# Kernel tuning notes

Measured on AMD Instinct MI355X. Metric: run time of the kernel, lower is better.

The kernel has to match this reference:

```python
import jax, jax.numpy as jnp
import numpy as np

B, L, H, D = 2, 2048, 16, 64
HID = H * D
EPS = 1e-6


def setup_inputs() -> dict:
    key = jax.random.key(0)
    k1, k2, k3 = jax.random.split(key, 3)
    x = jax.random.normal(k1, (B, L, HID), dtype=jnp.float32)
    Wqkv = jax.random.normal(k2, (HID, 3 * HID), dtype=jnp.float32) * 0.02
    Wo = jax.random.normal(k3, (HID, HID), dtype=jnp.float32) * 0.02
    q_norm_w = jnp.ones((D,), dtype=jnp.float32)
    k_norm_w = jnp.ones((D,), dtype=jnp.float32)
    # real RoPE tables: (L, D/2)
    d2 = D // 2
    inv_freq = 1.0 / (10000.0 ** (np.arange(d2, dtype=np.float32) / d2))
    ang = np.arange(L, dtype=np.float32)[:, None] * inv_freq[None, :]
    cos = jnp.asarray(np.cos(ang), dtype=jnp.float32)
    sin = jnp.asarray(np.sin(ang), dtype=jnp.float32)
    return {"x": x, "Wqkv": Wqkv, "Wo": Wo, "q_norm_w": q_norm_w,
            "k_norm_w": k_norm_w, "cos": cos, "sin": sin}


def _rmsnorm(t, w, eps=EPS):
    # normalize over last (head_dim) axis
    var = jnp.mean(t * t, axis=-1, keepdims=True)
    return t * jax.lax.rsqrt(var + eps) * w


def _rope(t, cos, sin):
    # t: (B,H,L,D); cos,sin: (1,1,L,D/2)
    d2 = t.shape[-1] // 2
    t1, t2 = t[..., :d2], t[..., d2:]
    return jnp.concatenate([t1 * cos - t2 * sin, t1 * sin + t2 * cos], axis=-1)


def reference(x, Wqkv, Wo, q_norm_w, k_norm_w, cos, sin):
    Bx, Lx, _ = x.shape
    qkv = x @ Wqkv                                   # (B,L,3*HID)
    qkv = qkv.reshape(Bx, Lx, 3, H, D)
    q = jnp.transpose(qkv[:, :, 0], (0, 2, 1, 3))    # (B,H,L,D)
    k = jnp.transpose(qkv[:, :, 1], (0, 2, 1, 3))
    v = jnp.transpose(qkv[:, :, 2], (0, 2, 1, 3))
    q = _rmsnorm(q, q_norm_w)
    k = _rmsnorm(k, k_norm_w)
    c = cos[:Lx][None, None]                         # (1,1,L,D/2)
    s = sin[:Lx][None, None]
    q = _rope(q, c, s)
    k = _rope(k, c, s)
    scale = 1.0 / jnp.sqrt(jnp.float32(D))
    scores = jnp.einsum("bhqd,bhkd->bhqk", q, k) * scale
    causal = jnp.tril(jnp.ones((Lx, Lx), dtype=bool))
    scores = jnp.where(causal, scores, jnp.finfo(scores.dtype).min)
    attn = jax.nn.softmax(scores, axis=-1)
    out = jnp.einsum("bhqk,bhkd->bhqd", attn, v)     # (B,H,L,D)
    out = jnp.transpose(out, (0, 2, 1, 3)).reshape(Bx, Lx, HID)
    return out @ Wo
```

## Files before the change

### kernel.cpp

```cpp
#include <hip/hip_runtime.h>
#include <hip/hip_bf16.h>

typedef __attribute__((ext_vector_type(8))) short bh8;
typedef __attribute__((ext_vector_type(4))) float f4;

typedef unsigned short u16;
typedef unsigned int u32;

__device__ inline u16 f2b(float f) {
  __hip_bfloat16 h = __float2bfloat16(f);
  union { __hip_bfloat16 h; u16 u; } v; v.h = h; return v.u;
}
__device__ inline float b2f(u16 b) {
  union { u32 u; float f; } v; v.u = ((u32)b) << 16;
  return v.f;
}

__device__ __forceinline__ void gload16(const u16* g, u16* l) {
  __builtin_amdgcn_global_load_lds(
      (__attribute__((address_space(1))) void*)(g),
      (__attribute__((address_space(3))) void*)(l),
      16, 0, 0);
}

__global__ __launch_bounds__(256) void k_prep1(const float* __restrict__ x,
                                               const float* __restrict__ Wqkv,
                                               const float* __restrict__ Wo,
                                               u16* __restrict__ xb,
                                               u16* __restrict__ wqkvT,
                                               u16* __restrict__ woT) {
  int idx = blockIdx.x;
  if (idx < 4096) {
    int i = (idx * 256 + threadIdx.x) * 4;
    float4 v = *(const float4*)&x[i];
    ushort4 o;
    o.x = f2b(v.x); o.y = f2b(v.y); o.z = f2b(v.z); o.w = f2b(v.w);
    *(ushort4*)&xb[i] = o;
    return;
  }
  __shared__ u16 t[32][33];
  const float* W; u16* WT; int K, N, bxi, byi;
  if (idx < 7168) {
    int id2 = idx - 4096;
    W = Wqkv; WT = wqkvT; K = 1024; N = 3072;
    bxi = id2 % 96; byi = id2 / 96;
  } else {
    int id2 = idx - 7168;
    W = Wo; WT = woT; K = 1024; N = 1024;
    bxi = id2 & 31; byi = id2 >> 5;
  }
  int bx = bxi * 32, by = byi * 32;
  int xx = threadIdx.x & 31, yy = threadIdx.x >> 5;
  for (int j = 0; j < 4; ++j) {
    int r = yy + j * 8;
    t[r][xx] = f2b(W[(size_t)(by + r) * N + bx + xx]);
  }
  __syncthreads();
  for (int j = 0; j < 4; ++j) {
    int r = yy + j * 8;
    WT[(size_t)(bx + r) * K + by + xx] = t[xx][r];
  }
}

template <bool F32OUT>
__global__ __launch_bounds__(256) void k_gemm(const u16* __restrict__ A,
                                              const u16* __restrict__ Bt,
                                              void* __restrict__ Cout,
                                              int M, int N, int K) {
  __shared__ u16 As[2][128 * 64];
  __shared__ u16 Bs[2][128 * 64];
  const int tid = threadIdx.x;
  const int lane = tid & 63, wid = tid >> 6;
  const int l15 = lane & 15, lg = lane >> 4;
  const int bm = blockIdx.x * 128, bn = blockIdx.y * 128;
  const int wr = (wid >> 1) * 64, wc = (wid & 1) * 64;

  f4 acc[4][4] = {};

  const int srow = wid * 32 + (lane >> 3);
  const int scol = (lane & 7) * 8;
  const u16* gA = A  + (size_t)(bm + srow) * K + scol;
  const u16* gB = Bt + (size_t)(bn + srow) * K + scol;

  const int nk = K >> 6;

  {
    const u16* ga = gA; const u16* gb = gB;
    u16* la = &As[0][(wid * 32) * 64];
    u16* lb = &Bs[0][(wid * 32) * 64];
    #pragma unroll
    for (int c = 0; c < 4; ++c) {
      gload16(ga, la);
      gload16(gb, lb);
      ga += (size_t)8 * K; gb += (size_t)8 * K;
      la += 8 * 64;        lb += 8 * 64;
    }
  }
  __syncthreads();

  for (int t = 0; t < nk; ++t) {
    if (t + 1 < nk) {
      int kb = (t + 1) << 6;
      const u16* ga = gA + kb; const u16* gb = gB + kb;
      u16* la = &As[(t + 1) & 1][(wid * 32) * 64];
      u16* lb = &Bs[(t + 1) & 1][(wid * 32) * 64];
      #pragma unroll
      for (int c = 0; c < 4; ++c) {
        gload16(ga, la);
        gload16(gb, lb);
        ga += (size_t)8 * K; gb += (size_t)8 * K;
        la += 8 * 64;        lb += 8 * 64;
      }
    }
    const u16* as = &As[t & 1][0];
    const u16* bs = &Bs[t & 1][0];
    #pragma unroll
    for (int kk = 0; kk < 2; ++kk) {
      bh8 a[4], b[4];
      #pragma unroll
      for (int m = 0; m < 4; ++m)
        a[m] = *(const bh8*)&as[(wr + m * 16 + l15) * 64 + kk * 32 + lg * 8];
      #pragma unroll
      for (int n = 0; n < 4; ++n)
        b[n] = *(const bh8*)&bs[(wc + n * 16 + l15) * 64 + kk * 32 + lg * 8];
      #pragma unroll
      for (int m = 0; m < 4; ++m)
        #pragma unroll
        for (int n = 0; n < 4; ++n)
          acc[m][n] = __builtin_amdgcn_mfma_f32_16x16x32_bf16(a[m], b[n], acc[m][n], 0, 0, 0);
    }
    __syncthreads();
  }

  for (int m = 0; m < 4; ++m)
    for (int n = 0; n < 4; ++n)
      for (int r = 0; r < 4; ++r) {
        int row = bm + wr + m * 16 + lg * 4 + r;
        int col = bn + wc + n * 16 + l15;
        float v = acc[m][n][r];
        if constexpr (F32OUT) ((float*)Cout)[(size_t)row * N + col] = v;
        else                  ((u16*)Cout)[(size_t)row * N + col]  = f2b(v);
      }
}

__global__ __launch_bounds__(256) void k_prep2(const u16* __restrict__ qkv,
                                               const float* __restrict__ qw,
                                               const float* __restrict__ kw,
                                               const float* __restrict__ cosp,
                                               const float* __restrict__ sinp,
                                               u16* __restrict__ Q,
                                               u16* __restrict__ K,
                                               u16* __restrict__ Vt) {
  const float CSC = 0.125f * 1.44269504088896f;
  int idx = blockIdx.x;
  if (idx < 2048) {
    int wid = threadIdx.x >> 6, lane = threadIdx.x & 63;
    int gw = idx * 4 + wid;
    int isK = gw & 1;
    int bl = gw >> 1;
    int l = bl & 2047, b = bl >> 11;
    int h = lane >> 2, qd = lane & 3;
    const u16* src = qkv + (size_t)bl * 3072 + isK * 1024 + h * 64 + qd * 8;
    bh8 t1 = *(const bh8*)src;
    bh8 t2 = *(const bh8*)(src + 32);
    float a1[8], a2[8];
    float ss = 0.0f;
    #pragma unroll
    for (int j = 0; j < 8; ++j) {
      a1[j] = b2f((u16)t1[j]); a2[j] = b2f((u16)t2[j]);
      ss += a1[j] * a1[j] + a2[j] * a2[j];
    }
    ss += __shfl_xor(ss, 1, 64);
    ss += __shfl_xor(ss, 2, 64);
    float rr = rsqrtf(ss * (1.0f / 64.0f) + 1e-6f);
    const float* wt = isK ? kw : qw;
    float w1[8], w2[8], cc[8], sn[8];
    *(float4*)&w1[0] = *(const float4*)&wt[qd * 8];
    *(float4*)&w1[4] = *(const float4*)&wt[qd * 8 + 4];
    *(float4*)&w2[0] = *(const float4*)&wt[32 + qd * 8];
    *(float4*)&w2[4] = *(const float4*)&wt[32 + qd * 8 + 4];
    *(float4*)&cc[0] = *(const float4*)&cosp[l * 32 + qd * 8];
    *(float4*)&cc[4] = *(const float4*)&cosp[l * 32 + qd * 8 + 4];
    *(float4*)&sn[0] = *(const float4*)&sinp[l * 32 + qd * 8];
    *(float4*)&sn[4] = *(const float4*)&sinp[l * 32 + qd * 8 + 4];
    float scl = isK ? 1.0f : CSC;
    bh8 o1, o2;
    #pragma unroll
    for (int j = 0; j < 8; ++j) {
      float x1 = a1[j] * rr * w1[j];
      float x2 = a2[j] * rr * w2[j];
      o1[j] = (short)f2b((x1 * cc[j] - x2 * sn[j]) * scl);
      o2[j] = (short)f2b((x1 * sn[j] + x2 * cc[j]) * scl);
    }
    u16* dst = (isK ? K : Q) + ((size_t)(b * 16 + h) * 2048 + l) * 64 + qd * 8;
    *(bh8*)dst = o1;
    *(bh8*)(dst + 32) = o2;
  } else {
    __shared__ u16 t[32][33];
    int v = idx - 2048;
    int bxi = v & 63, byi = (v >> 6) & 1, bh = v >> 7;
    int b = bh >> 4, h = bh & 15;
    int lb = bxi * 32, db = byi * 32;
    int xx = threadIdx.x & 31, yy = threadIdx.x >> 5;
    const u16* src = qkv + (size_t)b * 2048 * 3072 + 2048 + h * 64;
    for (int j = 0; j < 4; ++j) {
      int r = yy + j * 8;
      t[r][xx] = src[(size_t)(lb + r) * 3072 + db + xx];
    }
    __syncthreads();
    u16* dst = Vt + (size_t)bh * 64 * 2048;
    for (int j = 0; j < 4; ++j) {
      int r = yy + j * 8;
      dst[(size_t)(db + r) * 2048 + lb + xx] = t[xx][r];
    }
  }
}

__global__ __launch_bounds__(256, 4) void k_attn(const u16* __restrict__ Q,
                                                 const u16* __restrict__ K,
                                                 const u16* __restrict__ Vt,
                                                 u16* __restrict__ O,
                                                 u16* __restrict__ Opart,
                                                 float2* __restrict__ Ml) {
  __shared__ u16 Ks[2][64 * 64];
  __shared__ u16 Vs[2][64 * 64];

  const int bh = blockIdx.y;
  const int b = bh >> 4, h = bh & 15;
  const int wid = threadIdx.x >> 6, lane = threadIdx.x & 63;
  const int l15 = lane & 15, lg = lane >> 4;

  const int id = 39 - (int)blockIdx.x;
  int qt, t0, t1, slot;
  if (id < 4) { qt = id; t0 = 0; t1 = 2 * qt + 2; slot = -1; }
  else if (id < 12) {
    int p = id - 4; qt = 4 + (p >> 1); int half = p & 1;
    int nt = qt + 1; t0 = half * nt; t1 = t0 + nt;
    slot = bh * 36 + (qt - 4) * 2 + half;
  } else if (id < 24) {
    int p = id - 12; qt = 8 + p / 3; int part = p % 3;
    int T = 2 * qt + 2; t0 = part * T / 3; t1 = (part + 1) * T / 3;
    slot = bh * 36 + 8 + (qt - 8) * 3 + part;
  } else {
    int p = id - 24; qt = 12 + (p >> 2); int part = p & 3;
    int T = 2 * qt + 2; t0 = part * T / 4; t1 = (part + 1) * T / 4;
    slot = bh * 36 + 20 + (qt - 12) * 4 + part;
  }
  const int qb = qt * 128 + wid * 32;

  const u16* Qp = Q  + (size_t)bh * 2048 * 64;
  const u16* Kp = K  + (size_t)bh * 2048 * 64;
  const u16* Vp = Vt + (size_t)bh * 64 * 2048;

  const int sr0 = wid * 8 + (lane >> 3);
  const int sc  = lane & 7;

  bh8 aq[2][2];
  #pragma unroll
  for (int qi = 0; qi < 2; ++qi)
    #pragma unroll
    for (int hh = 0; hh < 2; ++hh)
      aq[qi][hh] = *(const bh8*)&Qp[(size_t)(qb + qi * 16 + l15) * 64 + hh * 32 + lg * 8];

  bh8 ones;
  #pragma unroll
  for (int j = 0; j < 8; ++j) ones[j] = (short)0x3F80;

  f4 acc[2][4] = {};
  float mrow[2] = {-1e30f, -1e30f};
  float lrow[2] = {0.0f, 0.0f};

  const int tmax = (qb + 31) >> 6;

  {
    int kb0 = t0 * 64;
    int r0 = sr0, r1 = 32 + sr0;
    gload16(Kp + (size_t)(kb0 + r0) * 64 + (size_t)((sc ^ (r0 & 7)) * 8), &Ks[t0 & 1][(wid * 8) * 64]);
    gload16(Kp + (size_t)(kb0 + r1) * 64 + (size_t)((sc ^ (r1 & 7)) * 8), &Ks[t0 & 1][(32 + wid * 8) * 64]);
    gload16(Vp + (size_t)r0 * 2048 + kb0 + (size_t)((sc ^ (r0 & 7)) * 8), &Vs[t0 & 1][(wid * 8) * 64]);
    gload16(Vp + (size_t)r1 * 2048 + kb0 + (size_t)((sc ^ (r1 & 7)) * 8), &Vs[t0 & 1][(32 + wid * 8) * 64]);
  }
  __syncthreads();

  for (int t = t0; t < t1; ++t) {
    if (t + 1 < t1) {
      int kb = (t + 1) * 64;
      int nb = (t + 1) & 1;
      int r0 = sr0, r1 = 32 + sr0;
      gload16(Kp + (size_t)(kb + r0) * 64 + (size_t)((sc ^ (r0 & 7)) * 8), &Ks[nb][(wid * 8) * 64]);
      gload16(Kp + (size_t)(kb + r1) * 64 + (size_t)((sc ^ (r1 & 7)) * 8), &Ks[nb][(32 + wid * 8) * 64]);
      gload16(Vp + (size_t)r0 * 2048 + kb + (size_t)((sc ^ (r0 & 7)) * 8), &Vs[nb][(wid * 8) * 64]);
      gload16(Vp + (size_t)r1 * 2048 + kb + (size_t)((sc ^ (r1 & 7)) * 8), &Vs[nb][(32 + wid * 8) * 64]);
    }
    if (t <= tmax) {
      const int kb = t * 64;
      const bool masked = (t == tmax);
      const u16* ks = &Ks[t & 1][0];
      const u16* vs = &Vs[t & 1][0];

      f4 sc4[4][2] = {};
      __builtin_amdgcn_s_setprio(1);
      #pragma unroll
      for (int kq = 0; kq < 4; ++kq) {
        int row = kq * 16 + l15;
        int cs = row & 7;
        bh8 ka0 = *(const bh8*)&ks[row * 64 + ((0 + lg) ^ cs) * 8];
        bh8 ka1 = *(const bh8*)&ks[row * 64 + ((4 + lg) ^ cs) * 8];
        #pragma unroll
        for (int qi = 0; qi < 2; ++qi) {
          sc4[kq][qi] = __builtin_amdgcn_mfma_f32_16x16x32_bf16(ka0, aq[qi][0], sc4[kq][qi], 0, 0, 0);
          sc4[kq][qi] = __builtin_amdgcn_mfma_f32_16x16x32_bf16(ka1, aq[qi][1], sc4[kq][qi], 0, 0, 0);
        }
      }
      __builtin_amdgcn_s_setprio(0);

      #pragma unroll
      for (int qi = 0; qi < 2; ++qi) {
        if (masked) {
          int q = qb + qi * 16 + l15;
          #pragma unroll
          for (int kq = 0; kq < 4; ++kq)
            #pragma unroll
            for (int r = 0; r < 4; ++r)
              if (kb + kq * 16 + lg * 4 + r > q) sc4[kq][qi][r] = -1e30f;
        }
        float mx = -1e30f;
        #pragma unroll
        for (int kq = 0; kq < 4; ++kq)
          #pragma unroll
          for (int r = 0; r < 4; ++r)
            mx = fmaxf(mx, sc4[kq][qi][r]);
        mx = fmaxf(mx, __shfl_xor(mx, 16, 64));
        mx = fmaxf(mx, __shfl_xor(mx, 32, 64));
        if (__any(mx > mrow[qi] + 8.0f)) {
          float mnew = fmaxf(mrow[qi], mx);
          float fac = exp2f(mrow[qi] - mnew);
          mrow[qi] = mnew;
          lrow[qi] *= fac;
          #pragma unroll
          for (int n = 0; n < 4; ++n)
            #pragma unroll
            for (int r = 0; r < 4; ++r) acc[qi][n][r] *= fac;
        }
        #pragma unroll
        for (int kq = 0; kq < 4; ++kq)
          #pragma unroll
          for (int r = 0; r < 4; ++r)
            sc4[kq][qi][r] = exp2f(sc4[kq][qi][r] - mrow[qi]);
      }

      bh8 pb[2][2];
      #pragma unroll
      for (int qi = 0; qi < 2; ++qi) {
        u32 W[8];
        #pragma unroll
        for (int kq = 0; kq < 4; ++kq) {
          W[kq * 2 + 0] = (u32)f2b(sc4[kq][qi][0]) | ((u32)f2b(sc4[kq][qi][1]) << 16);
          W[kq * 2 + 1] = (u32)f2b(sc4[kq][qi][2]) | ((u32)f2b(sc4[kq][qi][3]) << 16);
        }
        const bool b1 = (lg & 2) != 0, b0 = (lg & 1) != 0;
        u32 r0 = __shfl_xor(b1 ? W[0] : W[2], 32, 64);
        u32 r1 = __shfl_xor(b1 ? W[1] : W[3], 32, 64);
        u32 r2 = __shfl_xor(b1 ? W[4] : W[6], 32, 64);
        u32 r3 = __shfl_xor(b1 ? W[5] : W[7], 32, 64);
        u32 k0 = b1 ? W[2] : W[0];
        u32 k1 = b1 ? W[3] : W[1];
        u32 k2 = b1 ? W[6] : W[4];
        u32 k3 = b1 ? W[7] : W[5];
        const bool sr = (b1 == b0);
        u32 s0 = __shfl_xor(sr ? r0 : k0, 16, 64);
        u32 s1 = __shfl_xor(sr ? r1 : k1, 16, 64);
        u32 s2 = __shfl_xor(sr ? r2 : k2, 16, 64);
        u32 s3 = __shfl_xor(sr ? r3 : k3, 16, 64);
        union { u32 u[4]; bh8 v; } g0, g1;
        g0.u[0] = b0 ? s0 : (b1 ? r0 : k0);
        g0.u[1] = b0 ? s1 : (b1 ? r1 : k1);
        g0.u[2] = b0 ? (b1 ? k0 : r0) : s0;
        g0.u[3] = b0 ? (b1 ? k1 : r1) : s1;
        g1.u[0] = b0 ? s2 : (b1 ? r2 : k2);
        g1.u[1] = b0 ? s3 : (b1 ? r3 : k3);
        g1.u[2] = b0 ? (b1 ? k2 : r2) : s2;
        g1.u[3] = b0 ? (b1 ? k3 : r3) : s3;
        pb[0][qi] = g0.v;
        pb[1][qi] = g1.v;
      }

      f4 sum0 = {}, sum1 = {};
      __builtin_amdgcn_s_setprio(1);
      #pragma unroll
      for (int g = 0; g < 2; ++g) {
        #pragma unroll
        for (int n = 0; n < 4; ++n) {
          int row = n * 16 + l15;
          bh8 va = *(const bh8*)&vs[row * 64 + (((g * 4 + lg) ^ (row & 7)) * 8)];
          acc[0][n] = __builtin_amdgcn_mfma_f32_16x16x32_bf16(va, pb[g][0], acc[0][n], 0, 0, 0);
          acc[1][n] = __builtin_amdgcn_mfma_f32_16x16x32_bf16(va, pb[g][1], acc[1][n], 0, 0, 0);
        }
        sum0 = __builtin_amdgcn_mfma_f32_16x16x32_bf16(ones, pb[g][0], sum0, 0, 0, 0);
        sum1 = __builtin_amdgcn_mfma_f32_16x16x32_bf16(ones, pb[g][1], sum1, 0, 0, 0);
      }
      __builtin_amdgcn_s_setprio(0);
      lrow[0] += sum0[0];
      lrow[1] += sum1[0];
    }
    __syncthreads();
  }

  if (slot < 0) {
    #pragma unroll
    for (int qi = 0; qi < 2; ++qi) {
      float inv = 1.0f / lrow[qi];
      int q = qb + qi * 16 + l15;
      #pragma unroll
      for (int n = 0; n < 4; ++n) {
        ushort4 w4;
        w4.x = f2b(acc[qi][n][0] * inv);
        w4.y = f2b(acc[qi][n][1] * inv);
        w4.z = f2b(acc[qi][n][2] * inv);
        w4.w = f2b(acc[qi][n][3] * inv);
        *(ushort4*)&O[((size_t)b * 2048 + q) * 1024 + h * 64 + n * 16 + lg * 4] = w4;
      }
    }
  } else {
    u16* op = Opart + (size_t)slot * 8192;
    #pragma unroll
    for (int qi = 0; qi < 2; ++qi) {
      int rloc = wid * 32 + qi * 16 + l15;
      #pragma unroll
      for (int n = 0; n < 4; ++n) {
        ushort4 w4;
        w4.x = f2b(acc[qi][n][0]); w4.y = f2b(acc[qi][n][1]);
        w4.z = f2b(acc[qi][n][2]); w4.w = f2b(acc[qi][n][3]);
        *(ushort4*)&op[(size_t)rloc * 64 + n * 16 + lg * 4] = w4;
      }
      if (lg == 0) Ml[slot * 128 + rloc] = make_float2(mrow[qi], lrow[qi]);
    }
  }
}

__global__ __launch_bounds__(256) void k_comb(const u16* __restrict__ Opart,
                                              const float2* __restrict__ Ml,
                                              u16* __restrict__ O) {
  int qt = 4 + (int)blockIdx.x;
  int bh = blockIdx.y;
  int b = bh >> 4, h = bh & 15;
  int ways = qt < 8 ? 2 : (qt < 12 ? 3 : 4);
  int base = bh * 36 + (qt < 8 ? (qt - 4) * 2 : qt < 12 ? 8 + (qt - 8) * 3 : 20 + (qt - 12) * 4);
  int row = threadIdx.x >> 1;
  int db  = (threadIdx.x & 1) * 32;

  float2 ml[4]; float wgt[4];
  float M = -1e30f;
  #pragma unroll
  for (int w = 0; w < 4; ++w)
    if (w < ways) { ml[w] = Ml[(base + w) * 128 + row]; M = fmaxf(M, ml[w].x); }
  float l = 0.0f;
  #pragma unroll
  for (int w = 0; w < 4; ++w)
    if (w < ways) { wgt[w] = exp2f(ml[w].x - M); l += wgt[w] * ml[w].y; }
  float inv = 1.0f / l;

  u16* dst = O + ((size_t)b * 2048 + qt * 128 + row) * 1024 + h * 64 + db;
  #pragma unroll
  for (int j = 0; j < 32; j += 8) {
    float a[8] = {};
    #pragma unroll
    for (int w = 0; w < 4; ++w)
      if (w < ways) {
        bh8 v = *(const bh8*)&Opart[(size_t)(base + w) * 8192 + (size_t)row * 64 + db + j];
        #pragma unroll
        for (int e = 0; e < 8; ++e) a[e] += wgt[w] * b2f((u16)v[e]);
      }
    bh8 o;
    #pragma unroll
    for (int e = 0; e < 8; ++e) o[e] = (short)f2b(a[e] * inv);
    *(bh8*)&dst[j] = o;
  }
}

extern "C" void kernel_launch(void* const* d_in, const int* in_sizes, int n_in,
                              void* d_out, int out_size, void* d_ws, size_t ws_size,
                              hipStream_t stream) {
  (void)in_sizes; (void)n_in; (void)out_size; (void)ws_size;
  const float* x    = (const float*)d_in[0];
  const float* Wqkv = (const float*)d_in[1];
  const float* Wo   = (const float*)d_in[2];
  const float* qw   = (const float*)d_in[3];
  const float* kw   = (const float*)d_in[4];
  const float* cosp = (const float*)d_in[5];
  const float* sinp = (const float*)d_in[6];
  float* out = (float*)d_out;

  char* ws = (char*)d_ws;
  u16* xb    = (u16*)(ws);
  u16* wqkvT = (u16*)(ws + 8388608);
  u16* woT   = (u16*)(ws + 14680064);
  u16* qkv   = (u16*)(ws + 16777216);
  u16* Qb    = (u16*)(ws + 41943040);
  u16* Kb    = (u16*)(ws + 50331648);
  u16* Vtb   = (u16*)(ws + 58720256);
  u16* AO    = (u16*)(ws + 67108864);
  u16*    Opart = (u16*)(ws + 16777216);
  float2* Mlb   = (float2*)(ws + 35651584);

  k_prep1<<<8192, 256, 0, stream>>>(x, Wqkv, Wo, xb, wqkvT, woT);
  k_gemm<false><<<dim3(32, 24), 256, 0, stream>>>(xb, wqkvT, qkv, 4096, 3072, 1024);
  k_prep2<<<6144, 256, 0, stream>>>(qkv, qw, kw, cosp, sinp, Qb, Kb, Vtb);
  k_attn<<<dim3(40, 32), 256, 0, stream>>>(Qb, Kb, Vtb, AO, Opart, Mlb);
  k_comb<<<dim3(12, 32), 256, 0, stream>>>(Opart, Mlb, AO);
  k_gemm<true><<<dim3(32, 8), 256, 0, stream>>>(AO, woT, out, 4096, 1024, 1024);
}
```

Baseline: 154.0 us.

## Load K/V directly from global per wave and route P through per-wave LDS

Removes the shared double-buffered K/V LDS staging and block-wide barriers. Each wave now reads its K and V fragments straight from global memory. The P matrix moves from registers into MFMA operand layout through a per-wave swizzled LDS scratch instead of the shuffle network. The loop also ends at the last causal tile rather than iterating idle tiles up to the block's upper bound. This trades barrier and shuffle cost for four times the redundant global/L2 traffic across waves and exposed global load latency without prefetch.

```diff
diff --git a/kernel.cpp b/kernel.cpp
--- a/kernel.cpp
+++ b/kernel.cpp
@@ -222,8 +222,7 @@
                                                  u16* __restrict__ O,
                                                  u16* __restrict__ Opart,
                                                  float2* __restrict__ Ml) {
-  __shared__ u16 Ks[2][64 * 64];
-  __shared__ u16 Vs[2][64 * 64];
+  __shared__ u16 Pl[4][32][64];
 
   const int bh = blockIdx.y;
   const int b = bh >> 4, h = bh & 15;
@@ -252,9 +251,6 @@
   const u16* Kp = K  + (size_t)bh * 2048 * 64;
   const u16* Vp = Vt + (size_t)bh * 64 * 2048;
 
-  const int sr0 = wid * 8 + (lane >> 3);
-  const int sc  = lane & 7;
-
   bh8 aq[2][2];
   #pragma unroll
   for (int qi = 0; qi < 2; ++qi)
@@ -271,139 +267,97 @@
   float lrow[2] = {0.0f, 0.0f};
 
   const int tmax = (qb + 31) >> 6;
-
-  {
-    int kb0 = t0 * 64;
-    int r0 = sr0, r1 = 32 + sr0;
-    gload16(Kp + (size_t)(kb0 + r0) * 64 + (size_t)((sc ^ (r0 & 7)) * 8), &Ks[t0 & 1][(wid * 8) * 64]);
-    gload16(Kp + (size_t)(kb0 + r1) * 64 + (size_t)((sc ^ (r1 & 7)) * 8), &Ks[t0 & 1][(32 + wid * 8) * 64]);
-    gload16(Vp + (size_t)r0 * 2048 + kb0 + (size_t)((sc ^ (r0 & 7)) * 8), &Vs[t0 & 1][(wid * 8) * 64]);
-    gload16(Vp + (size_t)r1 * 2048 + kb0 + (size_t)((sc ^ (r1 & 7)) * 8), &Vs[t0 & 1][(32 + wid * 8) * 64]);
-  }
-  __syncthreads();
-
-  for (int t = t0; t < t1; ++t) {
-    if (t + 1 < t1) {
-      int kb = (t + 1) * 64;
-      int nb = (t + 1) & 1;
-      int r0 = sr0, r1 = 32 + sr0;
-      gload16(Kp + (size_t)(kb + r0) * 64 + (size_t)((sc ^ (r0 & 7)) * 8), &Ks[nb][(wid * 8) * 64]);
-      gload16(Kp + (size_t)(kb + r1) * 64 + (size_t)((sc ^ (r1 & 7)) * 8), &Ks[nb][(32 + wid * 8) * 64]);
-      gload16(Vp + (size_t)r0 * 2048 + kb + (size_t)((sc ^ (r0 & 7)) * 8), &Vs[nb][(wid * 8) * 64]);
-      gload16(Vp + (size_t)r1 * 2048 + kb + (size_t)((sc ^ (r1 & 7)) * 8), &Vs[nb][(32 + wid * 8) * 64]);
-    }
-    if (t <= tmax) {
-      const int kb = t * 64;
-      const bool masked = (t == tmax);
-      const u16* ks = &Ks[t & 1][0];
-      const u16* vs = &Vs[t & 1][0];
-
-      f4 sc4[4][2] = {};
-      __builtin_amdgcn_s_setprio(1);
-      #pragma unroll
-      for (int kq = 0; kq < 4; ++kq) {
-        int row = kq * 16 + l15;
-        int cs = row & 7;
-        bh8 ka0 = *(const bh8*)&ks[row * 64 + ((0 + lg) ^ cs) * 8];
-        bh8 ka1 = *(const bh8*)&ks[row * 64 + ((4 + lg) ^ cs) * 8];
-        #pragma unroll
-        for (int qi = 0; qi < 2; ++qi) {
-          sc4[kq][qi] = __builtin_amdgcn_mfma_f32_16x16x32_bf16(ka0, aq[qi][0], sc4[kq][qi], 0, 0, 0);
-          sc4[kq][qi] = __builtin_amdgcn_mfma_f32_16x16x32_bf16(ka1, aq[qi][1], sc4[kq][qi], 0, 0, 0);
-        }
-      }
-      __builtin_amdgcn_s_setprio(0);
-
+  const int tend = min(t1, tmax + 1);
+
+  char* plb = (char*)&Pl[wid][0][0];
+
+  for (int t = t0; t < tend; ++t) {
+    const int kb = t * 64;
+    const bool masked = (t == tmax);
+
+    f4 sc4[4][2] = {};
+    __builtin_amdgcn_s_setprio(1);
+    #pragma unroll
+    for (int kq = 0; kq < 4; ++kq) {
+      const u16* kr = &Kp[(size_t)(kb + kq * 16 + l15) * 64 + lg * 8];
+      bh8 ka0 = *(const bh8*)kr;
+      bh8 ka1 = *(const bh8*)(kr + 32);
       #pragma unroll
       for (int qi = 0; qi < 2; ++qi) {
-        if (masked) {
-          int q = qb + qi * 16 + l15;
-          #pragma unroll
-          for (int kq = 0; kq < 4; ++kq)
-            #pragma unroll
-            for (int r = 0; r < 4; ++r)
-              if (kb + kq * 16 + lg * 4 + r > q) sc4[kq][qi][r] = -1e30f;
-        }
-        float mx = -1e30f;
+        sc4[kq][qi] = __builtin_amdgcn_mfma_f32_16x16x32_bf16(ka0, aq[qi][0], sc4[kq][qi], 0, 0, 0);
+        sc4[kq][qi] = __builtin_amdgcn_mfma_f32_16x16x32_bf16(ka1, aq[qi][1], sc4[kq][qi], 0, 0, 0);
+      }
+    }
+    __builtin_amdgcn_s_setprio(0);
+
+    #pragma unroll
+    for (int qi = 0; qi < 2; ++qi) {
+      if (masked) {
+        int q = qb + qi * 16 + l15;
         #pragma unroll
         for (int kq = 0; kq < 4; ++kq)
           #pragma unroll
           for (int r = 0; r < 4; ++r)
-            mx = fmaxf(mx, sc4[kq][qi][r]);
-        mx = fmaxf(mx, __shfl_xor(mx, 16, 64));
-        mx = fmaxf(mx, __shfl_xor(mx, 32, 64));
-        if (__any(mx > mrow[qi] + 8.0f)) {
-          float mnew = fmaxf(mrow[qi], mx);
-          float fac = exp2f(mrow[qi] - mnew);
-          mrow[qi] = mnew;
-          lrow[qi] *= fac;
+            if (kb + kq * 16 + lg * 4 + r > q) sc4[kq][qi][r] = -1e30f;
+      }
+      float mx = -1e30f;
+      #pragma unroll
+      for (int kq = 0; kq < 4; ++kq)
+        #pragma unroll
+        for (int r = 0; r < 4; ++r)
+          mx = fmaxf(mx, sc4[kq][qi][r]);
+      mx = fmaxf(mx, __shfl_xor(mx, 16, 64));
+      mx = fmaxf(mx, __shfl_xor(mx, 32, 64));
+      if (__any(mx > mrow[qi] + 8.0f)) {
+        float mnew = fmaxf(mrow[qi], mx);
+        float fac = exp2f(mrow[qi] - mnew);
+        mrow[qi] = mnew;
+        lrow[qi] *= fac;
+        #pragma unroll
+        for (int n = 0; n < 4; ++n)
           #pragma unroll
-          for (int n = 0; n < 4; ++n)
-            #pragma unroll
-            for (int r = 0; r < 4; ++r) acc[qi][n][r] *= fac;
-        }
-        #pragma unroll
-        for (int kq = 0; kq < 4; ++kq)
-          #pragma unroll
-          for (int r = 0; r < 4; ++r)
-            sc4[kq][qi][r] = exp2f(sc4[kq][qi][r] - mrow[qi]);
-      }
-
-      bh8 pb[2][2];
-      #pragma unroll
-      for (int qi = 0; qi < 2; ++qi) {
-        u32 W[8];
-        #pragma unroll
-        for (int kq = 0; kq < 4; ++kq) {
-          W[kq * 2 + 0] = (u32)f2b(sc4[kq][qi][0]) | ((u32)f2b(sc4[kq][qi][1]) << 16);
-          W[kq * 2 + 1] = (u32)f2b(sc4[kq][qi][2]) | ((u32)f2b(sc4[kq][qi][3]) << 16);
-        }
-        const bool b1 = (lg & 2) != 0, b0 = (lg & 1) != 0;
-        u32 r0 = __shfl_xor(b1 ? W[0] : W[2], 32, 64);
-        u32 r1 = __shfl_xor(b1 ? W[1] : W[3], 32, 64);
-        u32 r2 = __shfl_xor(b1 ? W[4] : W[6], 32, 64);
-        u32 r3 = __shfl_xor(b1 ? W[5] : W[7], 32, 64);
-        u32 k0 = b1 ? W[2] : W[0];
-        u32 k1 = b1 ? W[3] : W[1];
-        u32 k2 = b1 ? W[6] : W[4];
-        u32 k3 = b1 ? W[7] : W[5];
-        const bool sr = (b1 == b0);
-        u32 s0 = __shfl_xor(sr ? r0 : k0, 16, 64);
-        u32 s1 = __shfl_xor(sr ? r1 : k1, 16, 64);
-        u32 s2 = __shfl_xor(sr ? r2 : k2, 16, 64);
-        u32 s3 = __shfl_xor(sr ? r3 : k3, 16, 64);
-        union { u32 u[4]; bh8 v; } g0, g1;
-        g0.u[0] = b0 ? s0 : (b1 ? r0 : k0);
-        g0.u[1] = b0 ? s1 : (b1 ? r1 : k1);
-        g0.u[2] = b0 ? (b1 ? k0 : r0) : s0;
-        g0.u[3] = b0 ? (b1 ? k1 : r1) : s1;
-        g1.u[0] = b0 ? s2 : (b1 ? r2 : k2);
-        g1.u[1] = b0 ? s3 : (b1 ? r3 : k3);
-        g1.u[2] = b0 ? (b1 ? k2 : r2) : s2;
-        g1.u[3] = b0 ? (b1 ? k3 : r3) : s3;
-        pb[0][qi] = g0.v;
-        pb[1][qi] = g1.v;
-      }
-
-      f4 sum0 = {}, sum1 = {};
-      __builtin_amdgcn_s_setprio(1);
-      #pragma unroll
-      for (int g = 0; g < 2; ++g) {
-        #pragma unroll
-        for (int n = 0; n < 4; ++n) {
-          int row = n * 16 + l15;
-          bh8 va = *(const bh8*)&vs[row * 64 + (((g * 4 + lg) ^ (row & 7)) * 8)];
-          acc[0][n] = __builtin_amdgcn_mfma_f32_16x16x32_bf16(va, pb[g][0], acc[0][n], 0, 0, 0);
-          acc[1][n] = __builtin_amdgcn_mfma_f32_16x16x32_bf16(va, pb[g][1], acc[1][n], 0, 0, 0);
-        }
-        sum0 = __builtin_amdgcn_mfma_f32_16x16x32_bf16(ones, pb[g][0], sum0, 0, 0, 0);
-        sum1 = __builtin_amdgcn_mfma_f32_16x16x32_bf16(ones, pb[g][1], sum1, 0, 0, 0);
-      }
-      __builtin_amdgcn_s_setprio(0);
-      lrow[0] += sum0[0];
-      lrow[1] += sum1[0];
-    }
-    __syncthreads();
+          for (int r = 0; r < 4; ++r) acc[qi][n][r] *= fac;
+      }
+      #pragma unroll
+      for (int kq = 0; kq < 4; ++kq)
+        #pragma unroll
+        for (int r = 0; r < 4; ++r)
+          sc4[kq][qi][r] = exp2f(sc4[kq][qi][r] - mrow[qi]);
+    }
+
+    #pragma unroll
+    for (int qi = 0; qi < 2; ++qi) {
+      int row = qi * 16 + l15;
+      #pragma unroll
+      for (int kq = 0; kq < 4; ++kq) {
+        ushort4 w4;
+        w4.x = f2b(sc4[kq][qi][0]); w4.y = f2b(sc4[kq][qi][1]);
+        w4.z = f2b(sc4[kq][qi][2]); w4.w = f2b(sc4[kq][qi][3]);
+        int ch = (kq * 2 + (lg >> 1)) ^ (row & 7);
+        *(ushort4*)(plb + row * 128 + ch * 16 + (lg & 1) * 8) = w4;
+      }
+    }
+    asm volatile("s_waitcnt lgkmcnt(0)" ::: "memory");
+    __builtin_amdgcn_sched_barrier(0);
+
+    f4 sum0 = {}, sum1 = {};
+    __builtin_amdgcn_s_setprio(1);
+    #pragma unroll
+    for (int g = 0; g < 2; ++g) {
+      bh8 pb0 = *(const bh8*)(plb + l15 * 128 + (((g * 4 + lg) ^ (l15 & 7)) * 16));
+      bh8 pb1 = *(const bh8*)(plb + (16 + l15) * 128 + (((g * 4 + lg) ^ (l15 & 7)) * 16));
+      #pragma unroll
+      for (int n = 0; n < 4; ++n) {
+        bh8 va = *(const bh8*)&Vp[(size_t)(n * 16 + l15) * 2048 + kb + g * 32 + lg * 8];
+        acc[0][n] = __builtin_amdgcn_mfma_f32_16x16x32_bf16(va, pb0, acc[0][n], 0, 0, 0);
+        acc[1][n] = __builtin_amdgcn_mfma_f32_16x16x32_bf16(va, pb1, acc[1][n], 0, 0, 0);
+      }
+      sum0 = __builtin_amdgcn_mfma_f32_16x16x32_bf16(ones, pb0, sum0, 0, 0, 0);
+      sum1 = __builtin_amdgcn_mfma_f32_16x16x32_bf16(ones, pb1, sum1, 0, 0, 0);
+    }
+    __builtin_amdgcn_s_setprio(0);
+    lrow[0] += sum0[0];
+    lrow[1] += sum1[0];
   }
 
   if (slot < 0) {
```

Measured after the change: 192.5 us. +25.0%, slower.
